# Kernel optimization log

Measured on AMD Instinct MI355X. Metric: run time of the kernel, lower is better.

## Reference

```python
import jax, jax.numpy as jnp
import numpy as np

G = 16          # grid_size
B = 2           # num graphs
SPACING = 1.5   # anchor_spacing
KA = 8          # atom_k_neighbors
KG = 24         # k_neighbors (grid->atom)
CUTOFF = 8.0
T = 16          # n_atom_types
H = 240         # hidden irreps dim (64x0e+32x1o+16x2e)
A = 9           # SH attr dim, lmax=2
C = 32          # code_dim
L = 2           # num_layers
BIG = 1e9

# real spherical harmonics, 'integral' normalization, e3nn component order
C0 = 0.28209479177387814   # 1/(2 sqrt(pi))
C1 = 0.4886025119029199    # sqrt(3/(4 pi))
C2A = 1.0925484305920792   # sqrt(15/(4 pi))
C2B = 0.31539156525252005  # sqrt(5/(16 pi))
C2C = 0.5462742152960396   # sqrt(15/(16 pi))

def _sph(rel, dist):
    u = rel / jnp.maximum(dist, 1e-9)[:, None]
    x, y, z = u[:, 0], u[:, 1], u[:, 2]
    return jnp.stack([
        jnp.full_like(x, C0),
        C1 * y, C1 * z, C1 * x,
        C2A * x * y, C2A * y * z, C2B * (3.0 * z * z - 1.0),
        C2A * z * x, C2C * (x * x - y * y),
    ], axis=-1)


def setup_inputs():
    key = jax.random.key(0)
    ks = jax.random.split(key, 12)
    Na = 1024
    half = G * SPACING / 2.0
    pos = jax.random.uniform(ks[0], (Na, 3), minval=-half, maxval=half, dtype=jnp.float32)
    atom_types = jax.random.randint(ks[1], (Na,), 0, T, dtype=jnp.int32)
    atom_batch = jnp.repeat(jnp.arange(B, dtype=jnp.int32), Na // B)

    def lin(k, shape):
        fan_in = shape[-2]
        return jax.random.normal(k, shape, dtype=jnp.float32) / jnp.sqrt(float(fan_in))

    Din = 2 * H + A
    return dict(
        pos=pos, atom_types=atom_types, atom_batch=atom_batch,
        We=lin(ks[2], (T + A, H)), be=jnp.zeros((H,), jnp.float32),
        Wm1=lin(ks[3], (L, Din, H)), bm1=jnp.zeros((L, H), jnp.float32),
        Wm2=lin(ks[4], (L, H, H)), bm2=jnp.zeros((L, H), jnp.float32),
        Wu1=lin(ks[5], (L, Din, H)), bu1=jnp.zeros((L, H), jnp.float32),
        Wu2=lin(ks[6], (L, H, H)), bu2=jnp.zeros((L, H), jnp.float32),
        Wo1=lin(ks[7], (H, H)), bo1=jnp.zeros((H,), jnp.float32),
        Wo2=lin(ks[8], (H, C)), bo2=jnp.zeros((C,), jnp.float32),
    )


def _forward(pos, atom_types, atom_batch, We, be, Wm1, bm1, Wm2, bm2,
             Wu1, bu1, Wu2, bu2, Wo1, bo1, Wo2, bo2):
    Na = pos.shape[0]
    ng = G ** 3
    Ng = B * ng
    N = Na + Ng

    # anchor grid, centered, spacing SPACING
    ax = (jnp.arange(G, dtype=pos.dtype) - (G - 1) / 2.0) * SPACING
    grid = jnp.stack(jnp.meshgrid(ax, ax, ax, indexing='ij'), -1).reshape(-1, 3)  # [ng,3]
    grid_flat = jnp.tile(grid, (B, 1))                                            # [Ng,3]
    grid_batch = jnp.repeat(jnp.arange(B, dtype=atom_batch.dtype), ng)
    node_pos = jnp.concatenate([pos, grid_flat], 0)                               # [N,3]

    # atom-atom knn_graph (no self loops, per-graph)
    d2 = jnp.sum((pos[:, None] - pos[None]) ** 2, -1)                             # [Na,Na]
    d2 = jnp.where(atom_batch[:, None] == atom_batch[None], d2, BIG)
    d2 = jnp.where(jnp.eye(Na, dtype=bool), BIG, d2)
    _, nbr = jax.lax.top_k(-d2, KA)                                               # [Na,KA]

    # grid->atom knn (per-graph), edge src=atom, dst=grid node
    d2g = jnp.sum((grid_flat[:, None] - pos[None]) ** 2, -1)                      # [Ng,Na]
    d2g = jnp.where(grid_batch[:, None] == atom_batch[None], d2g, BIG)
    _, nbg = jax.lax.top_k(-d2g, KG)                                              # [Ng,KG]

    src = jnp.concatenate([nbr.reshape(-1), nbg.reshape(-1)])
    dst = jnp.concatenate([jnp.repeat(jnp.arange(Na), KA),
                           Na + jnp.repeat(jnp.arange(Ng), KG)])

    rel = node_pos[src] - node_pos[dst]
    dist = jnp.linalg.norm(rel, axis=-1)
    mask = (dist <= CUTOFF).astype(pos.dtype)        # cutoff as mask (jit-friendly)
    ea = _sph(rel, dist) * mask[:, None]             # [E,A]

    # node attrs: scatter-mean of edge SH over destination nodes
    na_sum = jax.ops.segment_sum(ea, dst, num_segments=N)
    cnt = jax.ops.segment_sum(mask, dst, num_segments=N)
    node_attr = na_sum / jnp.maximum(cnt, 1.0)[:, None]
    node_attr = node_attr.at[:, 0].set(1.0)

    # node features: one-hot atoms, zeros for anchors
    feat = jnp.concatenate([jax.nn.one_hot(atom_types, T, dtype=pos.dtype),
                            jnp.zeros((Ng, T), pos.dtype)], 0)
    h = jax.nn.silu(jnp.concatenate([feat, node_attr], -1) @ We + be)

    # SEGNN-style message passing (attr-conditioned MLPs, masked-sum aggregation)
    for l in range(L):
        mi = jnp.concatenate([h[src], h[dst], ea], -1)                            # [E,2H+A]
        m = jax.nn.silu(jax.nn.silu(mi @ Wm1[l] + bm1[l]) @ Wm2[l] + bm2[l])
        m = m * mask[:, None]
        agg = jax.ops.segment_sum(m, dst, num_segments=N)                         # [N,H]
        ui = jnp.concatenate([h, agg, node_attr], -1)                             # [N,2H+A]
        h = h + jax.nn.silu(jax.nn.silu(ui @ Wu1[l] + bu1[l]) @ Wu2[l] + bu2[l])

    out = jax.nn.silu(h @ Wo1 + bo1) @ Wo2 + bo2                                  # [N,C]
    return out[Na:].reshape(B, ng, C)


def reference(pos, atom_types, atom_batch, We, be, Wm1, bm1, Wm2, bm2,
              Wu1, bu1, Wu2, bu2, Wo1, bo1, Wo2, bo2):
    return _forward(pos, atom_types, atom_batch, We, be, Wm1, bm1, Wm2, bm2,
                    Wu1, bu1, Wu2, bu2, Wo1, bo1, Wo2, bo2)
```

## Files before the change

kernel.cpp:

```cpp
#include <hip/hip_runtime.h>
#include <math.h>

#define NA   1024
#define NGRID 4096
#define NB   2
#define NG   (NB*NGRID)
#define NN   (NA+NG)
#define KAK  8
#define KGK  24
#define EAE  (NA*KAK)
#define EGE  (NG*KGK)
#define ET   (EAE+EGE)
#define HD   240
#define TT   16
#define DIN  489
#define CD   32
#define CUTF 8.0f

typedef __attribute__((ext_vector_type(8))) short short8;
typedef __attribute__((ext_vector_type(4))) short short4v;
typedef __attribute__((ext_vector_type(4))) float f32x4;

__device__ __forceinline__ float silu_f(float x) {
    return x / (1.0f + __expf(-x));
}
__device__ __forceinline__ short f2bf(float x) {
    unsigned u = __float_as_uint(x);
    unsigned r = (u + 0x7FFFu + ((u >> 16) & 1u)) >> 16;
    return (short)r;
}

template <int K>
__device__ __forceinline__ void wave_topk(unsigned long long key[8], int lane,
                                          int* __restrict__ outp) {
    unsigned long long lmin = key[0];
#pragma unroll
    for (int s = 1; s < 8; ++s) lmin = key[s] < lmin ? key[s] : lmin;
    int myout = -1;
    for (int t = 0; t < K; ++t) {
        unsigned long long m = lmin;
#pragma unroll
        for (int d = 1; d < 64; d <<= 1) {
            unsigned long long o = __shfl_xor(m, d);
            m = o < m ? o : m;
        }
        if (lane == t) myout = (int)(m & 1023u);
        if (m == lmin) {
#pragma unroll
            for (int s = 0; s < 8; ++s) if (key[s] == m) key[s] = ~0ull;
            lmin = key[0];
#pragma unroll
            for (int s = 1; s < 8; ++s) lmin = key[s] < lmin ? key[s] : lmin;
        }
    }
    if (lane < K) outp[lane] = myout;
}

__global__ __launch_bounds__(256) void knn_atoms_kernel(const float* __restrict__ pos,
                                                        int* __restrict__ nbr) {
    __shared__ float sx[512], sy[512], sz[512];
    int tid = threadIdx.x;
    int q0 = blockIdx.x * 4;
    int pbase = (q0 >= 512) ? 512 : 0;
    for (int j = tid; j < 512; j += 256) {
        sx[j] = pos[(pbase + j)*3 + 0];
        sy[j] = pos[(pbase + j)*3 + 1];
        sz[j] = pos[(pbase + j)*3 + 2];
    }
    __syncthreads();
    int lane = tid & 63;
    int i = q0 + (tid >> 6);
    float px = sx[i - pbase], py = sy[i - pbase], pz = sz[i - pbase];
    unsigned long long key[8];
#pragma unroll
    for (int s = 0; s < 8; ++s) {
        int c = s * 64 + lane;
        int j = pbase + c;
        float dx = px - sx[c], dy = py - sy[c], dz = pz - sz[c];
        float d2 = __fadd_rn(__fadd_rn(__fmul_rn(dx,dx), __fmul_rn(dy,dy)), __fmul_rn(dz,dz));
        key[s] = ((unsigned long long)__float_as_uint(d2) << 10) | (unsigned)j;
        if (j == i) key[s] = ~0ull;
    }
    wave_topk<KAK>(key, lane, &nbr[i*KAK]);
}

__global__ __launch_bounds__(256) void knn_grid_kernel(const float* __restrict__ pos,
                                                       int* __restrict__ nbg) {
    __shared__ float sx[512], sy[512], sz[512];
    int tid = threadIdx.x;
    int q0 = blockIdx.x * 4;
    int pbase = (q0 >= NGRID) ? 512 : 0;
    for (int j = tid; j < 512; j += 256) {
        sx[j] = pos[(pbase + j)*3 + 0];
        sy[j] = pos[(pbase + j)*3 + 1];
        sz[j] = pos[(pbase + j)*3 + 2];
    }
    __syncthreads();
    int lane = tid & 63;
    int g = q0 + (tid >> 6);
    int gi = g & (NGRID - 1);
    int ix = gi >> 8, iy = (gi >> 4) & 15, iz = gi & 15;
    float px = ((float)ix - 7.5f) * 1.5f;
    float py = ((float)iy - 7.5f) * 1.5f;
    float pz = ((float)iz - 7.5f) * 1.5f;
    unsigned long long key[8];
#pragma unroll
    for (int s = 0; s < 8; ++s) {
        int c = s * 64 + lane;
        int j = pbase + c;
        float dx = px - sx[c], dy = py - sy[c], dz = pz - sz[c];
        float d2 = __fadd_rn(__fadd_rn(__fmul_rn(dx,dx), __fmul_rn(dy,dy)), __fmul_rn(dz,dz));
        key[s] = ((unsigned long long)__float_as_uint(d2) << 10) | (unsigned)j;
    }
    wave_topk<KGK>(key, lane, &nbg[g*KGK]);
}

__global__ void edge_kernel(const float* __restrict__ pos, const int* __restrict__ nbr,
                            const int* __restrict__ nbg, float* __restrict__ ea,
                            float* __restrict__ emask) {
    int e = blockIdx.x * blockDim.x + threadIdx.x;
    if (e >= ET) return;
    int src; float dpx, dpy, dpz;
    if (e < EAE) {
        int d = e >> 3;
        src = nbr[e];
        dpx = pos[d*3]; dpy = pos[d*3+1]; dpz = pos[d*3+2];
    } else {
        int eg = e - EAE;
        src = nbg[eg];
        int gg = eg / KGK;
        int gi = gg % NGRID;
        int ix = gi >> 8, iy = (gi >> 4) & 15, iz = gi & 15;
        dpx = ((float)ix - 7.5f) * 1.5f;
        dpy = ((float)iy - 7.5f) * 1.5f;
        dpz = ((float)iz - 7.5f) * 1.5f;
    }
    float rx = pos[src*3] - dpx, ry = pos[src*3+1] - dpy, rz = pos[src*3+2] - dpz;
    float dist = sqrtf(rx*rx + ry*ry + rz*rz);
    float mask = (dist <= CUTF) ? 1.0f : 0.0f;
    float inv = 1.0f / fmaxf(dist, 1e-9f);
    float x = rx * inv, y = ry * inv, z = rz * inv;
    float s0 = 0.28209479177387814f;
    float s1 = 0.4886025119029199f * y;
    float s2 = 0.4886025119029199f * z;
    float s3 = 0.4886025119029199f * x;
    float s4 = 1.0925484305920792f * x * y;
    float s5 = 1.0925484305920792f * y * z;
    float s6 = 0.31539156525252005f * (3.0f * z * z - 1.0f);
    float s7 = 1.0925484305920792f * z * x;
    float s8 = 0.5462742152960396f * (x * x - y * y);
    float* o = &ea[(size_t)e * 9];
    o[0] = s0 * mask; o[1] = s1 * mask; o[2] = s2 * mask; o[3] = s3 * mask;
    o[4] = s4 * mask; o[5] = s5 * mask; o[6] = s6 * mask; o[7] = s7 * mask; o[8] = s8 * mask;
    emask[e] = mask;
}

__global__ void node_attr_kernel(const float* __restrict__ ea, const float* __restrict__ emask,
                                 float* __restrict__ attr) {
    int n = blockIdx.x * blockDim.x + threadIdx.x;
    if (n >= NN) return;
    int K, e0;
    if (n < NA) { K = KAK; e0 = n * KAK; }
    else        { K = KGK; e0 = EAE + (n - NA) * KGK; }
    float s[9];
#pragma unroll
    for (int a = 0; a < 9; ++a) s[a] = 0.f;
    float cnt = 0.f;
    for (int k = 0; k < K; ++k) {
        cnt += emask[e0 + k];
        const float* p = &ea[(size_t)(e0 + k) * 9];
#pragma unroll
        for (int a = 0; a < 9; ++a) s[a] += p[a];
    }
    float invc = 1.0f / fmaxf(cnt, 1.0f);
    attr[n*9+0] = 1.0f;
#pragma unroll
    for (int a = 1; a < 9; ++a) attr[n*9+a] = s[a] * invc;
}

__global__ void encoder_kernel(const int* __restrict__ types, const float* __restrict__ attr,
                               const float* __restrict__ We, const float* __restrict__ be,
                               float* __restrict__ h) {
    int idx = blockIdx.x * blockDim.x + threadIdx.x;
    int n = idx / HD, j = idx % HD;
    float acc = be[j];
    if (n < NA) acc += We[types[n] * HD + j];
#pragma unroll
    for (int a = 0; a < 9; ++a) acc += attr[n*9+a] * We[(TT + a) * HD + j];
    h[idx] = silu_f(acc);
}

__global__ void convert_w_kernel(const float* __restrict__ src, short* __restrict__ dst,
                                 int K, int Kpad) {
    int idx = blockIdx.x * blockDim.x + threadIdx.x;
    int per = 256 * Kpad;
    int l = idx / per;
    int rem = idx % per;
    int col = rem / Kpad, k = rem % Kpad;
    short v = 0;
    if (k < K && col < 240) v = f2bf(src[(size_t)l * K * 240 + (size_t)k * 240 + col]);
    dst[idx] = v;
}

__global__ void node_z_kernel(const float* __restrict__ h, const float* __restrict__ Wm1,
                              const float* __restrict__ bm1,
                              float* __restrict__ Zs, float* __restrict__ Zd) {
    const int NBT = 8;
    __shared__ float hs[NBT*HD];
    int tid = threadIdx.x;
    int n0 = blockIdx.x * NBT;
    for (int idx = tid; idx < NBT*HD; idx += 256)
        hs[idx] = h[(size_t)n0*HD + idx];
    __syncthreads();
    int j = tid;
    if (j >= HD) return;
    if (n0 < NA) {
        float zd[NBT], zs[NBT];
        float b = bm1[j];
#pragma unroll
        for (int k = 0; k < NBT; ++k) { zd[k] = b; zs[k] = 0.f; }
        for (int i = 0; i < HD; ++i) {
            float wd = Wm1[(240 + i)*HD + j];
            float ws = Wm1[i*HD + j];
#pragma unroll
            for (int k = 0; k < NBT; ++k) {
                float hv = hs[k*HD + i];
                zd[k] += hv * wd;
                zs[k] += hv * ws;
            }
        }
#pragma unroll
        for (int k = 0; k < NBT; ++k) {
            Zd[(size_t)(n0 + k)*HD + j] = zd[k];
            Zs[(size_t)(n0 + k)*HD + j] = zs[k];
        }
    } else {
        float zd[NBT];
        float b = bm1[j];
#pragma unroll
        for (int k = 0; k < NBT; ++k) zd[k] = b;
        for (int i = 0; i < HD; ++i) {
            float wd = Wm1[(240 + i)*HD + j];
#pragma unroll
            for (int k = 0; k < NBT; ++k) zd[k] += hs[k*HD + i] * wd;
        }
#pragma unroll
        for (int k = 0; k < NBT; ++k) Zd[(size_t)(n0 + k)*HD + j] = zd[k];
    }
}

__global__ __launch_bounds__(256) void msg_gemm_kernel(
        const float* __restrict__ Zs, const float* __restrict__ Zd,
        const int* __restrict__ nbg, const float* __restrict__ ea,
        const float* __restrict__ emask, const float* __restrict__ Wea,
        const short* __restrict__ wm2t, const float* __restrict__ bm2,
        float* __restrict__ agg) {
    __shared__ __align__(16) short Abuf[96 * 256];
    __shared__ __align__(16) float mkbuf[96];
    int tid = threadIdx.x;
    int blk = blockIdx.x;
    int e0 = blk * 96;

#pragma unroll
    for (int it = 0; it < 12; ++it) {
        int idx = it * 256 + tid;
        int row = idx >> 5, q = idx & 31;
        short8 o = {0,0,0,0,0,0,0,0};
        if (q < 30) {
            int j = q * 8;
            int eg = e0 + row;
            int srcn = nbg[eg];
            int dstn = NA + blk * 4 + row / KGK;
            const float4 zs0 = *(const float4*)(Zs + (size_t)srcn * HD + j);
            const float4 zs1 = *(const float4*)(Zs + (size_t)srcn * HD + j + 4);
            const float4 zd0 = *(const float4*)(Zd + (size_t)dstn * HD + j);
            const float4 zd1 = *(const float4*)(Zd + (size_t)dstn * HD + j + 4);
            float s0 = zs0.x + zd0.x, s1 = zs0.y + zd0.y, s2 = zs0.z + zd0.z, s3 = zs0.w + zd0.w;
            float s4 = zs1.x + zd1.x, s5 = zs1.y + zd1.y, s6 = zs1.z + zd1.z, s7 = zs1.w + zd1.w;
            const float* ep = ea + (size_t)(EAE + eg) * 9;
#pragma unroll
            for (int a = 0; a < 9; ++a) {
                float ev = ep[a];
                const float4 w0 = *(const float4*)(Wea + a * HD + j);
                const float4 w1 = *(const float4*)(Wea + a * HD + j + 4);
                s0 += ev * w0.x; s1 += ev * w0.y; s2 += ev * w0.z; s3 += ev * w0.w;
                s4 += ev * w1.x; s5 += ev * w1.y; s6 += ev * w1.z; s7 += ev * w1.w;
            }
            o[0] = f2bf(silu_f(s0)); o[1] = f2bf(silu_f(s1));
            o[2] = f2bf(silu_f(s2)); o[3] = f2bf(silu_f(s3));
            o[4] = f2bf(silu_f(s4)); o[5] = f2bf(silu_f(s5));
            o[6] = f2bf(silu_f(s6)); o[7] = f2bf(silu_f(s7));
        }
        *(short8*)((char*)Abuf + row * 512 + ((q * 16) ^ ((row & 7) << 4))) = o;
    }
    if (tid < 96) mkbuf[tid] = emask[EAE + e0 + tid];
    __syncthreads();

    int wid = tid >> 6, lane = tid & 63;
    int mw = wid >> 1, nw = wid & 1;
    int lg = lane >> 4, lc = lane & 15;
    int rbase = mw * 48;
    int col0 = nw * 128;

    f32x4 acc[3][8];
#pragma unroll
    for (int mt = 0; mt < 3; ++mt)
#pragma unroll
        for (int nt = 0; nt < 8; ++nt) acc[mt][nt] = (f32x4){0.f, 0.f, 0.f, 0.f};

#pragma unroll
    for (int kc = 0; kc < 8; ++kc) {
        short8 af[3];
#pragma unroll
        for (int mt = 0; mt < 3; ++mt)
            af[mt] = *(const short8*)&Abuf[(rbase + mt*16 + lc) * 256 +
                                           ((kc*32 + lg*8) ^ ((lc & 7) << 3))];
#pragma unroll
        for (int nt = 0; nt < 8; ++nt) {
            const short8 bf = *(const short8*)(wm2t + (size_t)(col0 + nt*16 + lc) * 256 + kc*32 + lg*8);
#pragma unroll
            for (int mt = 0; mt < 3; ++mt)
                acc[mt][nt] = __builtin_amdgcn_mfma_f32_16x16x32_bf16(af[mt], bf, acc[mt][nt], 0, 0, 0);
        }
    }

#pragma unroll
    for (int nt = 0; nt < 8; ++nt) {
        int ncol = col0 + nt * 16 + lc;
        float bias = (ncol < HD) ? bm2[ncol] : 0.f;
        float p[3];
#pragma unroll
        for (int mt = 0; mt < 3; ++mt) {
            const float4 mkv = *(const float4*)&mkbuf[rbase + mt*16 + lg*4];
            float t0 = silu_f(acc[mt][nt].x + bias) * mkv.x;
            float t1 = silu_f(acc[mt][nt].y + bias) * mkv.y;
            float t2 = silu_f(acc[mt][nt].z + bias) * mkv.z;
            float t3 = silu_f(acc[mt][nt].w + bias) * mkv.w;
            p[mt] = (t0 + t1) + (t2 + t3);
        }
        float v0 = p[0] + ((lg < 2) ? p[1] : 0.f);
        float v1 = ((lg >= 2) ? p[1] : 0.f) + p[2];
        v0 += __shfl_xor(v0, 16); v0 += __shfl_xor(v0, 32);
        v1 += __shfl_xor(v1, 16); v1 += __shfl_xor(v1, 32);
        if (ncol < HD) {
            int node = NA + blk * 4 + mw * 2;
            if (lane < 16)      agg[(size_t)(node + 0) * HD + ncol] = v0;
            else if (lane < 32) agg[(size_t)(node + 1) * HD + ncol] = v1;
        }
    }
}

template <int KE, int NPB>
__global__ __launch_bounds__(192) void msg_mfma_kernel(
        const float* __restrict__ Zs, const float* __restrict__ Zd,
        const int* __restrict__ nbrList, const float* __restrict__ ea,
        const float* __restrict__ emask, const float* __restrict__ Wea,
        const short* __restrict__ wm2t, const float* __restrict__ bm2,
        float* __restrict__ agg, int dstBase, int edgeBase) {
    constexpr int ROWS = KE * NPB;
    constexpr int MT = ROWS / 16;
    __shared__ __align__(16) short Abuf[ROWS * 264];
    __shared__ __align__(16) float mkbuf[ROWS];

    int tid = threadIdx.x;
    int b = blockIdx.x;
    int e0 = edgeBase + b * ROWS;

    if (tid < ROWS) mkbuf[tid] = emask[e0 + tid];
    for (int idx = tid; idx < ROWS * 24; idx += 192) {
        int r = idx / 24;
        Abuf[r * 264 + 240 + (idx % 24)] = 0;
    }
    for (int idx = tid; idx < ROWS * 60; idx += 192) {
        int row = idx / 60;
        int j = (idx % 60) * 4;
        int srcn = nbrList[b * ROWS + row];
        int dstn = dstBase + b * NPB + row / KE;
        const float4 zs = *(const float4*)(Zs + (size_t)srcn * HD + j);
        const float4 zd = *(const float4*)(Zd + (size_t)dstn * HD + j);
        float s0 = zs.x + zd.x, s1 = zs.y + zd.y, s2 = zs.z + zd.z, s3 = zs.w + zd.w;
        const float* ep = ea + (size_t)(e0 + row) * 9;
#pragma unroll
        for (int a = 0; a < 9; ++a) {
            float ev = ep[a];
            const float4 w = *(const float4*)(Wea + a * HD + j);
            s0 += ev * w.x; s1 += ev * w.y; s2 += ev * w.z; s3 += ev * w.w;
        }
        short4v o;
        o.x = f2bf(silu_f(s0)); o.y = f2bf(silu_f(s1));
        o.z = f2bf(silu_f(s2)); o.w = f2bf(silu_f(s3));
        *(short4v*)&Abuf[row * 264 + j] = o;
    }
    __syncthreads();

    int w = tid / 64, lane = tid % 64;
    int lg = lane >> 4, lc = lane & 15;
    int wcol0 = w * 80;

    f32x4 acc[MT][5];
#pragma unroll
    for (int mt = 0; mt < MT; ++mt)
#pragma unroll
        for (int nt = 0; nt < 5; ++nt) acc[mt][nt] = (f32x4){0.f, 0.f, 0.f, 0.f};

#pragma unroll
    for (int kc = 0; kc < 8; ++kc) {
        short8 af[MT];
#pragma unroll
        for (int mt = 0; mt < MT; ++mt)
            af[mt] = *(const short8*)&Abuf[(mt * 16 + lc) * 264 + kc * 32 + lg * 8];
#pragma unroll
        for (int nt = 0; nt < 5; ++nt) {
            const short8 bf = *(const short8*)(wm2t + (size_t)(wcol0 + nt * 16 + lc) * 256 + kc * 32 + lg * 8);
#pragma unroll
            for (int mt = 0; mt < MT; ++mt)
                acc[mt][nt] = __builtin_amdgcn_mfma_f32_16x16x32_bf16(af[mt], bf, acc[mt][nt], 0, 0, 0);
        }
    }

#pragma unroll
    for (int nt = 0; nt < 5; ++nt) {
        int ncol = wcol0 + nt * 16 + lc;
        float bias = bm2[ncol];
        float p[MT];
#pragma unroll
        for (int mt = 0; mt < MT; ++mt) {
            const float4 mkv = *(const float4*)&mkbuf[mt * 16 + lg * 4];
            float t0 = silu_f(acc[mt][nt].x + bias) * mkv.x;
            float t1 = silu_f(acc[mt][nt].y + bias) * mkv.y;
            float t2 = silu_f(acc[mt][nt].z + bias) * mkv.z;
            float t3 = silu_f(acc[mt][nt].w + bias) * mkv.w;
            p[mt] = (t0 + t1) + (t2 + t3);
        }
#pragma unroll
        for (int mt = 0; mt < MT; ++mt) {
            float v = p[mt];
            v += __shfl_xor(v, 16);
            if (lane < 16)
                agg[(size_t)(dstBase + b * (2 * MT) + 2 * mt + 0) * HD + ncol] = v;
            else if (lane >= 32 && lane < 48)
                agg[(size_t)(dstBase + b * (2 * MT) + 2 * mt + 1) * HD + ncol] = v;
        }
    }
}

__global__ __launch_bounds__(256) void update_mfma_kernel(
        float* __restrict__ h, const float* __restrict__ agg,
        const float* __restrict__ attr,
        const short* __restrict__ wu1t, const float* __restrict__ bu1,
        const short* __restrict__ wu2t, const float* __restrict__ bu2) {
    __shared__ __align__(16) short Abuf[32 * 512];
    __shared__ __align__(16) short Ubuf[32 * 256];
    int tid = threadIdx.x;
    int n0 = blockIdx.x * 32;

#pragma unroll
    for (int it = 0; it < 8; ++it) {
        int idx = it * 256 + tid;
        int row = idx >> 6, q = idx & 63;
        int j = q * 8;
        int n = n0 + row;
        short8 o = {0,0,0,0,0,0,0,0};
        if (j < 240) {
            const float4 a0 = *(const float4*)(h + (size_t)n * HD + j);
            const float4 a1 = *(const float4*)(h + (size_t)n * HD + j + 4);
            o[0]=f2bf(a0.x); o[1]=f2bf(a0.y); o[2]=f2bf(a0.z); o[3]=f2bf(a0.w);
            o[4]=f2bf(a1.x); o[5]=f2bf(a1.y); o[6]=f2bf(a1.z); o[7]=f2bf(a1.w);
        } else if (j < 480) {
            const float4 a0 = *(const float4*)(agg + (size_t)n * HD + (j - 240));
            const float4 a1 = *(const float4*)(agg + (size_t)n * HD + (j - 240) + 4);
            o[0]=f2bf(a0.x); o[1]=f2bf(a0.y); o[2]=f2bf(a0.z); o[3]=f2bf(a0.w);
            o[4]=f2bf(a1.x); o[5]=f2bf(a1.y); o[6]=f2bf(a1.z); o[7]=f2bf(a1.w);
        } else if (j == 480) {
#pragma unroll
            for (int a = 0; a < 8; ++a) o[a] = f2bf(attr[n*9 + a]);
        } else if (j == 488) {
            o[0] = f2bf(attr[n*9 + 8]);
        }
        *(short8*)((char*)Abuf + row * 1024 + ((q * 16) ^ ((row & 7) << 4))) = o;
    }
    __syncthreads();

    int wid = tid >> 6, lane = tid & 63;
    int mw = wid >> 1, nw = wid & 1;
    int lg = lane >> 4, lc = lane & 15;
    int col0 = nw * 128;

    f32x4 acc[8];
#pragma unroll
    for (int nt = 0; nt < 8; ++nt) acc[nt] = (f32x4){0.f, 0.f, 0.f, 0.f};
#pragma unroll
    for (int kc = 0; kc < 16; ++kc) {
        const short8 af = *(const short8*)((char*)Abuf + (mw*16 + lc) * 1024 +
                                           ((kc*64 + lg*16) ^ ((lc & 7) << 4)));
#pragma unroll
        for (int nt = 0; nt < 8; ++nt) {
            const short8 bf = *(const short8*)(wu1t + (size_t)(col0 + nt*16 + lc) * 512 + kc*32 + lg*8);
            acc[nt] = __builtin_amdgcn_mfma_f32_16x16x32_bf16(af, bf, acc[nt], 0, 0, 0);
        }
    }
#pragma unroll
    for (int nt = 0; nt < 8; ++nt) {
        int ncol = col0 + nt * 16 + lc;
        float bias = (ncol < HD) ? bu1[ncol] : 0.f;
        float vals[4] = {acc[nt].x, acc[nt].y, acc[nt].z, acc[nt].w};
#pragma unroll
        for (int r = 0; r < 4; ++r) {
            int row = mw*16 + lg*4 + r;
            *(short*)((char*)Ubuf + row * 512 + ((ncol * 2) ^ ((row & 7) << 4))) =
                f2bf(silu_f(vals[r] + bias));
        }
    }
    __syncthreads();

    f32x4 acc2[8];
#pragma unroll
    for (int nt = 0; nt < 8; ++nt) acc2[nt] = (f32x4){0.f, 0.f, 0.f, 0.f};
#pragma unroll
    for (int kc = 0; kc < 8; ++kc) {
        const short8 af = *(const short8*)((char*)Ubuf + (mw*16 + lc) * 512 +
                                           ((kc*64 + lg*16) ^ ((lc & 7) << 4)));
#pragma unroll
        for (int nt = 0; nt < 8; ++nt) {
            const short8 bf = *(const short8*)(wu2t + (size_t)(col0 + nt*16 + lc) * 256 + kc*32 + lg*8);
            acc2[nt] = __builtin_amdgcn_mfma_f32_16x16x32_bf16(af, bf, acc2[nt], 0, 0, 0);
        }
    }
#pragma unroll
    for (int nt = 0; nt < 8; ++nt) {
        int ncol = col0 + nt * 16 + lc;
        if (ncol < HD) {
            float bias = bu2[ncol];
            float vals[4] = {acc2[nt].x, acc2[nt].y, acc2[nt].z, acc2[nt].w};
#pragma unroll
            for (int r = 0; r < 4; ++r) {
                int row = mw*16 + lg*4 + r;
                size_t hi = (size_t)(n0 + row) * HD + ncol;
                h[hi] += silu_f(vals[r] + bias);
            }
        }
    }
}

__global__ void output_kernel(const float* __restrict__ h,
                              const float* __restrict__ Wo1, const float* __restrict__ bo1,
                              const float* __restrict__ Wo2, const float* __restrict__ bo2,
                              float* __restrict__ out) {
    const int NBT = 4;
    __shared__ float hr[NBT][HD];
    __shared__ float o1[NBT][HD];
    int tid = threadIdx.x;
    int g0 = blockIdx.x * NBT;
    for (int idx = tid; idx < NBT * HD; idx += 256) {
        int k = idx / HD, i = idx % HD;
        hr[k][i] = h[(size_t)(NA + g0 + k) * HD + i];
    }
    __syncthreads();
    int j = tid;
    if (j < HD) {
        float acc[NBT] = {0.f, 0.f, 0.f, 0.f};
        for (int i4 = 0; i4 < 60; ++i4) {
            int i = 4 * i4;
            float w0 = Wo1[(i+0)*HD+j], w1 = Wo1[(i+1)*HD+j];
            float w2 = Wo1[(i+2)*HD+j], w3 = Wo1[(i+3)*HD+j];
#pragma unroll
            for (int k = 0; k < NBT; ++k) {
                const float4 a = *reinterpret_cast<const float4*>(&hr[k][i]);
                acc[k] += a.x*w0 + a.y*w1 + a.z*w2 + a.w*w3;
            }
        }
        float bb = bo1[j];
#pragma unroll
        for (int k = 0; k < NBT; ++k) o1[k][j] = silu_f(acc[k] + bb);
    }
    __syncthreads();
    if (tid < NBT * CD) {
        int k = tid >> 5, c = tid & 31;
        float acc = bo2[c];
        for (int i = 0; i < HD; ++i) acc += o1[k][i] * Wo2[i*CD + c];
        out[(size_t)(g0 + k) * CD + c] = acc;
    }
}

extern "C" void kernel_launch(void* const* d_in, const int* in_sizes, int n_in,
                              void* d_out, int out_size, void* d_ws, size_t ws_size,
                              hipStream_t stream) {
    (void)in_sizes; (void)n_in; (void)out_size; (void)ws_size;
    const float* pos   = (const float*)d_in[0];
    const int*   types = (const int*)d_in[1];
    const int*   batch = (const int*)d_in[2];
    (void)batch;
    const float* We    = (const float*)d_in[3];
    const float* be    = (const float*)d_in[4];
    const float* Wm1   = (const float*)d_in[5];
    const float* bm1   = (const float*)d_in[6];
    const float* Wm2   = (const float*)d_in[7];
    const float* bm2   = (const float*)d_in[8];
    const float* Wu1   = (const float*)d_in[9];
    const float* bu1   = (const float*)d_in[10];
    const float* Wu2   = (const float*)d_in[11];
    const float* bu2   = (const float*)d_in[12];
    const float* Wo1   = (const float*)d_in[13];
    const float* bo1   = (const float*)d_in[14];
    const float* Wo2   = (const float*)d_in[15];
    const float* bo2   = (const float*)d_in[16];
    float* out = (float*)d_out;

    char* ws = (char*)d_ws;
    size_t off = 0;
    auto take = [&](size_t bytes) -> char* {
        char* p = ws + off;
        off = (off + bytes + 255) & ~(size_t)255;
        return p;
    };
    int*   nbr   = (int*)take((size_t)EAE * 4);
    int*   nbg   = (int*)take((size_t)EGE * 4);
    float* ea    = (float*)take((size_t)ET * 9 * 4);
    float* emask = (float*)take((size_t)ET * 4);
    float* attr  = (float*)take((size_t)NN * 9 * 4);
    float* h     = (float*)take((size_t)NN * HD * 4);
    float* agg   = (float*)take((size_t)NN * HD * 4);
    float* zs    = (float*)take((size_t)NA * HD * 4);
    float* zd    = (float*)take((size_t)NN * HD * 4);
    short* wm2t  = (short*)take((size_t)2 * 256 * 256 * 2);
    short* wu1t  = (short*)take((size_t)2 * 256 * 512 * 2);
    short* wu2t  = (short*)take((size_t)2 * 256 * 256 * 2);

    knn_atoms_kernel<<<NA/4, 256, 0, stream>>>(pos, nbr);
    knn_grid_kernel<<<NG/4, 256, 0, stream>>>(pos, nbg);
    edge_kernel<<<ET/256, 256, 0, stream>>>(pos, nbr, nbg, ea, emask);
    node_attr_kernel<<<NN/256, 256, 0, stream>>>(ea, emask, attr);
    encoder_kernel<<<(NN*HD)/256, 256, 0, stream>>>(types, attr, We, be, h);
    convert_w_kernel<<<(2*256*256)/256, 256, 0, stream>>>(Wm2, wm2t, 240, 256);
    convert_w_kernel<<<(2*256*512)/256, 256, 0, stream>>>(Wu1, wu1t, DIN, 512);
    convert_w_kernel<<<(2*256*256)/256, 256, 0, stream>>>(Wu2, wu2t, 240, 256);

    for (int l = 0; l < 2; ++l) {
        const float* wm1 = Wm1 + (size_t)l * DIN * HD;
        const float* bb1 = bm1 + l * HD;
        const float* wea = wm1 + (size_t)480 * HD;
        const short* w2t = wm2t + (size_t)l * 256 * 256;
        const float* bb2 = bm2 + l * HD;
        node_z_kernel<<<NN/8, 256, 0, stream>>>(h, wm1, bb1, zs, zd);
        msg_mfma_kernel<KAK, 8><<<NA*KAK/64, 192, 0, stream>>>(
            zs, zd, nbr, ea, emask, wea, w2t, bb2, agg, 0, 0);
        msg_gemm_kernel<<<EGE/96, 256, 0, stream>>>(zs, zd, nbg, ea, emask, wea, w2t, bb2, agg);
        update_mfma_kernel<<<NN/32, 256, 0, stream>>>(
            h, agg, attr,
            wu1t + (size_t)l * 256 * 512, bu1 + l * HD,
            wu2t + (size_t)l * 256 * 256, bu2 + l * HD);
    }
    output_kernel<<<NG/4, 256, 0, stream>>>(h, Wo1, bo1, Wo2, bo2, out);
}
```

Before: 673.0 us.

## Move node Z projection to split-bf16 MFMA and halve msg_gemm block tile

Replaces the scalar FP32 node_z kernel with an MFMA kernel. It splits activations and weights into bf16 hi/lo pairs and runs three MFMAs per tile (hi*hi, hi*lo, lo*hi) to keep close to fp32 accuracy, with new conversion kernels preparing the hi/lo weight copies. Separately, msg_gemm now handles 48 edges (2 grid nodes) per block instead of 96, each wave covering 64 columns. This doubles the block count and lowers LDS and register use, at the cost of reading more weight traffic per edge.

```diff
diff --git a/kernel.cpp b/kernel.cpp
--- a/kernel.cpp
+++ b/kernel.cpp
@@ -28,6 +28,9 @@
     unsigned u = __float_as_uint(x);
     unsigned r = (u + 0x7FFFu + ((u >> 16) & 1u)) >> 16;
     return (short)r;
+}
+__device__ __forceinline__ float bf2f(short s) {
+    return __uint_as_float(((unsigned)(unsigned short)s) << 16);
 }
 
 template <int K>
@@ -202,50 +205,117 @@
     dst[idx] = v;
 }
 
-__global__ void node_z_kernel(const float* __restrict__ h, const float* __restrict__ Wm1,
-                              const float* __restrict__ bm1,
-                              float* __restrict__ Zs, float* __restrict__ Zd) {
-    const int NBT = 8;
-    __shared__ float hs[NBT*HD];
+__global__ void convert_wm1hl_kernel(const float* __restrict__ Wm1, short* __restrict__ hi,
+                                     short* __restrict__ lo, int rowoff) {
+    int idx = blockIdx.x * blockDim.x + threadIdx.x;
+    int l = idx >> 16;
+    int rem = idx & 65535;
+    int col = rem >> 8, k = rem & 255;
+    float v = 0.f;
+    if (k < 240 && col < 240) v = Wm1[(size_t)l * DIN * HD + (size_t)(rowoff + k) * HD + col];
+    short h16 = f2bf(v);
+    hi[idx] = h16;
+    lo[idx] = f2bf(v - bf2f(h16));
+}
+
+__global__ __launch_bounds__(256) void node_z_mfma_kernel(
+        const float* __restrict__ h,
+        const short* __restrict__ wzd_hi, const short* __restrict__ wzd_lo,
+        const short* __restrict__ wzs_hi, const short* __restrict__ wzs_lo,
+        const float* __restrict__ bm1,
+        float* __restrict__ Zs, float* __restrict__ Zd) {
+    __shared__ __align__(16) short Ahi[32 * 256];
+    __shared__ __align__(16) short Alo[32 * 256];
     int tid = threadIdx.x;
-    int n0 = blockIdx.x * NBT;
-    for (int idx = tid; idx < NBT*HD; idx += 256)
-        hs[idx] = h[(size_t)n0*HD + idx];
-    __syncthreads();
-    int j = tid;
-    if (j >= HD) return;
+    int n0 = blockIdx.x * 32;
+
+#pragma unroll
+    for (int it = 0; it < 4; ++it) {
+        int idx = it * 256 + tid;
+        int row = idx >> 5, q = idx & 31;
+        int j = q * 8;
+        short8 ohi = {0,0,0,0,0,0,0,0}, olo = {0,0,0,0,0,0,0,0};
+        if (j < 240) {
+            const float4 a0 = *(const float4*)(h + (size_t)(n0 + row) * HD + j);
+            const float4 a1 = *(const float4*)(h + (size_t)(n0 + row) * HD + j + 4);
+            float v[8] = {a0.x, a0.y, a0.z, a0.w, a1.x, a1.y, a1.z, a1.w};
+#pragma unroll
+            for (int a = 0; a < 8; ++a) {
+                short hh = f2bf(v[a]);
+                ohi[a] = hh;
+                olo[a] = f2bf(v[a] - bf2f(hh));
+            }
+        }
+        int boff = row * 512 + ((q * 16) ^ ((row & 7) << 4));
+        *(short8*)((char*)Ahi + boff) = ohi;
+        *(short8*)((char*)Alo + boff) = olo;
+    }
+    __syncthreads();
+
+    int wid = tid >> 6, lane = tid & 63;
+    int mw = wid >> 1, nw = wid & 1;
+    int lg = lane >> 4, lc = lane & 15;
+    int col0 = nw * 128;
+    int arow = (mw * 16 + lc) * 256;
+
+    f32x4 acc[8];
+#pragma unroll
+    for (int nt = 0; nt < 8; ++nt) acc[nt] = (f32x4){0.f, 0.f, 0.f, 0.f};
+#pragma unroll
+    for (int kc = 0; kc < 8; ++kc) {
+        int aoff = arow + ((kc * 32 + lg * 8) ^ ((lc & 7) << 3));
+        const short8 ahi = *(const short8*)&Ahi[aoff];
+        const short8 alo = *(const short8*)&Alo[aoff];
+#pragma unroll
+        for (int nt = 0; nt < 8; ++nt) {
+            size_t bo = (size_t)(col0 + nt*16 + lc) * 256 + kc*32 + lg*8;
+            const short8 bhi = *(const short8*)(wzd_hi + bo);
+            const short8 blo = *(const short8*)(wzd_lo + bo);
+            acc[nt] = __builtin_amdgcn_mfma_f32_16x16x32_bf16(ahi, bhi, acc[nt], 0, 0, 0);
+            acc[nt] = __builtin_amdgcn_mfma_f32_16x16x32_bf16(ahi, blo, acc[nt], 0, 0, 0);
+            acc[nt] = __builtin_amdgcn_mfma_f32_16x16x32_bf16(alo, bhi, acc[nt], 0, 0, 0);
+        }
+    }
+#pragma unroll
+    for (int nt = 0; nt < 8; ++nt) {
+        int ncol = col0 + nt * 16 + lc;
+        if (ncol < HD) {
+            float bias = bm1[ncol];
+            float vals[4] = {acc[nt].x, acc[nt].y, acc[nt].z, acc[nt].w};
+#pragma unroll
+            for (int r = 0; r < 4; ++r)
+                Zd[(size_t)(n0 + mw*16 + lg*4 + r) * HD + ncol] = vals[r] + bias;
+        }
+    }
+
     if (n0 < NA) {
-        float zd[NBT], zs[NBT];
-        float b = bm1[j];
-#pragma unroll
-        for (int k = 0; k < NBT; ++k) { zd[k] = b; zs[k] = 0.f; }
-        for (int i = 0; i < HD; ++i) {
-            float wd = Wm1[(240 + i)*HD + j];
-            float ws = Wm1[i*HD + j];
-#pragma unroll
-            for (int k = 0; k < NBT; ++k) {
-                float hv = hs[k*HD + i];
-                zd[k] += hv * wd;
-                zs[k] += hv * ws;
+#pragma unroll
+        for (int nt = 0; nt < 8; ++nt) acc[nt] = (f32x4){0.f, 0.f, 0.f, 0.f};
+#pragma unroll
+        for (int kc = 0; kc < 8; ++kc) {
+            int aoff = arow + ((kc * 32 + lg * 8) ^ ((lc & 7) << 3));
+            const short8 ahi = *(const short8*)&Ahi[aoff];
+            const short8 alo = *(const short8*)&Alo[aoff];
+#pragma unroll
+            for (int nt = 0; nt < 8; ++nt) {
+                size_t bo = (size_t)(col0 + nt*16 + lc) * 256 + kc*32 + lg*8;
+                const short8 bhi = *(const short8*)(wzs_hi + bo);
+                const short8 blo = *(const short8*)(wzs_lo + bo);
+                acc[nt] = __builtin_amdgcn_mfma_f32_16x16x32_bf16(ahi, bhi, acc[nt], 0, 0, 0);
+                acc[nt] = __builtin_amdgcn_mfma_f32_16x16x32_bf16(ahi, blo, acc[nt], 0, 0, 0);
+                acc[nt] = __builtin_amdgcn_mfma_f32_16x16x32_bf16(alo, bhi, acc[nt], 0, 0, 0);
             }
         }
 #pragma unroll
-        for (int k = 0; k < NBT; ++k) {
-            Zd[(size_t)(n0 + k)*HD + j] = zd[k];
-            Zs[(size_t)(n0 + k)*HD + j] = zs[k];
-        }
-    } else {
-        float zd[NBT];
-        float b = bm1[j];
-#pragma unroll
-        for (int k = 0; k < NBT; ++k) zd[k] = b;
-        for (int i = 0; i < HD; ++i) {
-            float wd = Wm1[(240 + i)*HD + j];
-#pragma unroll
-            for (int k = 0; k < NBT; ++k) zd[k] += hs[k*HD + i] * wd;
-        }
-#pragma unroll
-        for (int k = 0; k < NBT; ++k) Zd[(size_t)(n0 + k)*HD + j] = zd[k];
+        for (int nt = 0; nt < 8; ++nt) {
+            int ncol = col0 + nt * 16 + lc;
+            if (ncol < HD) {
+                float vals[4] = {acc[nt].x, acc[nt].y, acc[nt].z, acc[nt].w};
+#pragma unroll
+                for (int r = 0; r < 4; ++r)
+                    Zs[(size_t)(n0 + mw*16 + lg*4 + r) * HD + ncol] = vals[r];
+            }
+        }
     }
 }
 
@@ -255,14 +325,14 @@
         const float* __restrict__ emask, const float* __restrict__ Wea,
         const short* __restrict__ wm2t, const float* __restrict__ bm2,
         float* __restrict__ agg) {
-    __shared__ __align__(16) short Abuf[96 * 256];
-    __shared__ __align__(16) float mkbuf[96];
+    __shared__ __align__(16) short Abuf[48 * 256];
+    __shared__ __align__(16) float mkbuf[48];
     int tid = threadIdx.x;
     int blk = blockIdx.x;
-    int e0 = blk * 96;
-
-#pragma unroll
-    for (int it = 0; it < 12; ++it) {
+    int e0 = blk * 48;
+
+#pragma unroll
+    for (int it = 0; it < 6; ++it) {
         int idx = it * 256 + tid;
         int row = idx >> 5, q = idx & 31;
         short8 o = {0,0,0,0,0,0,0,0};
@@ -270,7 +340,7 @@
             int j = q * 8;
             int eg = e0 + row;
             int srcn = nbg[eg];
-            int dstn = NA + blk * 4 + row / KGK;
+            int dstn = NA + blk * 2 + row / KGK;
             const float4 zs0 = *(const float4*)(Zs + (size_t)srcn * HD + j);
             const float4 zs1 = *(const float4*)(Zs + (size_t)srcn * HD + j + 4);
             const float4 zd0 = *(const float4*)(Zd + (size_t)dstn * HD + j);
@@ -293,30 +363,28 @@
         }
         *(short8*)((char*)Abuf + row * 512 + ((q * 16) ^ ((row & 7) << 4))) = o;
     }
-    if (tid < 96) mkbuf[tid] = emask[EAE + e0 + tid];
+    if (tid < 48) mkbuf[tid] = emask[EAE + e0 + tid];
     __syncthreads();
 
     int wid = tid >> 6, lane = tid & 63;
-    int mw = wid >> 1, nw = wid & 1;
     int lg = lane >> 4, lc = lane & 15;
-    int rbase = mw * 48;
-    int col0 = nw * 128;
-
-    f32x4 acc[3][8];
+    int col0 = wid * 64;
+
+    f32x4 acc[3][4];
 #pragma unroll
     for (int mt = 0; mt < 3; ++mt)
 #pragma unroll
-        for (int nt = 0; nt < 8; ++nt) acc[mt][nt] = (f32x4){0.f, 0.f, 0.f, 0.f};
+        for (int nt = 0; nt < 4; ++nt) acc[mt][nt] = (f32x4){0.f, 0.f, 0.f, 0.f};
 
 #pragma unroll
     for (int kc = 0; kc < 8; ++kc) {
         short8 af[3];
 #pragma unroll
         for (int mt = 0; mt < 3; ++mt)
-            af[mt] = *(const short8*)&Abuf[(rbase + mt*16 + lc) * 256 +
+            af[mt] = *(const short8*)&Abuf[(mt*16 + lc) * 256 +
                                            ((kc*32 + lg*8) ^ ((lc & 7) << 3))];
 #pragma unroll
-        for (int nt = 0; nt < 8; ++nt) {
+        for (int nt = 0; nt < 4; ++nt) {
             const short8 bf = *(const short8*)(wm2t + (size_t)(col0 + nt*16 + lc) * 256 + kc*32 + lg*8);
 #pragma unroll
             for (int mt = 0; mt < 3; ++mt)
@@ -325,13 +393,13 @@
     }
 
 #pragma unroll
-    for (int nt = 0; nt < 8; ++nt) {
+    for (int nt = 0; nt < 4; ++nt) {
         int ncol = col0 + nt * 16 + lc;
         float bias = (ncol < HD) ? bm2[ncol] : 0.f;
         float p[3];
 #pragma unroll
         for (int mt = 0; mt < 3; ++mt) {
-            const float4 mkv = *(const float4*)&mkbuf[rbase + mt*16 + lg*4];
+            const float4 mkv = *(const float4*)&mkbuf[mt*16 + lg*4];
             float t0 = silu_f(acc[mt][nt].x + bias) * mkv.x;
             float t1 = silu_f(acc[mt][nt].y + bias) * mkv.y;
             float t2 = silu_f(acc[mt][nt].z + bias) * mkv.z;
@@ -343,7 +411,7 @@
         v0 += __shfl_xor(v0, 16); v0 += __shfl_xor(v0, 32);
         v1 += __shfl_xor(v1, 16); v1 += __shfl_xor(v1, 32);
         if (ncol < HD) {
-            int node = NA + blk * 4 + mw * 2;
+            int node = NA + blk * 2;
             if (lane < 16)      agg[(size_t)(node + 0) * HD + ncol] = v0;
             else if (lane < 32) agg[(size_t)(node + 1) * HD + ncol] = v1;
         }
@@ -613,18 +681,22 @@
         off = (off + bytes + 255) & ~(size_t)255;
         return p;
     };
-    int*   nbr   = (int*)take((size_t)EAE * 4);
-    int*   nbg   = (int*)take((size_t)EGE * 4);
-    float* ea    = (float*)take((size_t)ET * 9 * 4);
-    float* emask = (float*)take((size_t)ET * 4);
-    float* attr  = (float*)take((size_t)NN * 9 * 4);
-    float* h     = (float*)take((size_t)NN * HD * 4);
-    float* agg   = (float*)take((size_t)NN * HD * 4);
-    float* zs    = (float*)take((size_t)NA * HD * 4);
-    float* zd    = (float*)take((size_t)NN * HD * 4);
-    short* wm2t  = (short*)take((size_t)2 * 256 * 256 * 2);
-    short* wu1t  = (short*)take((size_t)2 * 256 * 512 * 2);
-    short* wu2t  = (short*)take((size_t)2 * 256 * 256 * 2);
+    int*   nbr    = (int*)take((size_t)EAE * 4);
+    int*   nbg    = (int*)take((size_t)EGE * 4);
+    float* ea     = (float*)take((size_t)ET * 9 * 4);
+    float* emask  = (float*)take((size_t)ET * 4);
+    float* attr   = (float*)take((size_t)NN * 9 * 4);
+    float* h      = (float*)take((size_t)NN * HD * 4);
+    float* agg    = (float*)take((size_t)NN * HD * 4);
+    float* zs     = (float*)take((size_t)NA * HD * 4);
+    float* zd     = (float*)take((size_t)NN * HD * 4);
+    short* wm2t   = (short*)take((size_t)2 * 256 * 256 * 2);
+    short* wu1t   = (short*)take((size_t)2 * 256 * 512 * 2);
+    short* wu2t   = (short*)take((size_t)2 * 256 * 256 * 2);
+    short* wzd_hi = (short*)take((size_t)2 * 256 * 256 * 2);
+    short* wzd_lo = (short*)take((size_t)2 * 256 * 256 * 2);
+    short* wzs_hi = (short*)take((size_t)2 * 256 * 256 * 2);
+    short* wzs_lo = (short*)take((size_t)2 * 256 * 256 * 2);
 
     knn_atoms_kernel<<<NA/4, 256, 0, stream>>>(pos, nbr);
     knn_grid_kernel<<<NG/4, 256, 0, stream>>>(pos, nbg);
@@ -634,17 +706,22 @@
     convert_w_kernel<<<(2*256*256)/256, 256, 0, stream>>>(Wm2, wm2t, 240, 256);
     convert_w_kernel<<<(2*256*512)/256, 256, 0, stream>>>(Wu1, wu1t, DIN, 512);
     convert_w_kernel<<<(2*256*256)/256, 256, 0, stream>>>(Wu2, wu2t, 240, 256);
+    convert_wm1hl_kernel<<<(2*256*256)/256, 256, 0, stream>>>(Wm1, wzd_hi, wzd_lo, 240);
+    convert_wm1hl_kernel<<<(2*256*256)/256, 256, 0, stream>>>(Wm1, wzs_hi, wzs_lo, 0);
 
     for (int l = 0; l < 2; ++l) {
         const float* wm1 = Wm1 + (size_t)l * DIN * HD;
-        const float* bb1 = bm1 + l * HD;
         const float* wea = wm1 + (size_t)480 * HD;
         const short* w2t = wm2t + (size_t)l * 256 * 256;
         const float* bb2 = bm2 + l * HD;
-        node_z_kernel<<<NN/8, 256, 0, stream>>>(h, wm1, bb1, zs, zd);
+        node_z_mfma_kernel<<<NN/32, 256, 0, stream>>>(
+            h,
+            wzd_hi + (size_t)l * 65536, wzd_lo + (size_t)l * 65536,
+            wzs_hi + (size_t)l * 65536, wzs_lo + (size_t)l * 65536,
+            bm1 + l * HD, zs, zd);
         msg_mfma_kernel<KAK, 8><<<NA*KAK/64, 192, 0, stream>>>(
             zs, zd, nbr, ea, emask, wea, w2t, bb2, agg, 0, 0);
-        msg_gemm_kernel<<<EGE/96, 256, 0, stream>>>(zs, zd, nbg, ea, emask, wea, w2t, bb2, agg);
+        msg_gemm_kernel<<<EGE/48, 256, 0, stream>>>(zs, zd, nbg, ea, emask, wea, w2t, bb2, agg);
         update_mfma_kernel<<<NN/32, 256, 0, stream>>>(
             h, agg, attr,
             wu1t + (size_t)l * 256 * 512, bu1 + l * HD,
```

Result: slower. 696.4 us (+3.5%).
